# Kernel tuning notes

Hardware: AMD Instinct MI355X
Metric: run time of the kernel (lower is better)

Reference implementation:

```python
import jax, jax.numpy as jnp
import numpy as np

B, D_IN, H, LAT = 4096, 4096, 4096, 512


def setup_inputs() -> dict:
    key = jax.random.key(0)
    ks = jax.random.split(key, 10)
    s = lambda fan_in: 1.0 / np.sqrt(fan_in)
    return {
        "x": jax.random.normal(ks[0], (B, D_IN), jnp.float32),
        "W_e1": jax.random.normal(ks[1], (D_IN, H), jnp.float32) * s(D_IN),
        "b_e1": jax.random.uniform(ks[2], (H,), jnp.float32),
        "W_e2": jax.random.normal(ks[3], (H, 2 * LAT), jnp.float32) * s(H),
        "b_e2": jax.random.uniform(ks[4], (2 * LAT,), jnp.float32),
        "W_d1": jax.random.normal(ks[5], (LAT, H), jnp.float32) * s(LAT),
        "b_d1": jax.random.uniform(ks[6], (H,), jnp.float32),
        "W_d2": jax.random.normal(ks[7], (H, D_IN), jnp.float32) * s(H),
        "b_d2": jax.random.uniform(ks[8], (D_IN,), jnp.float32),
        "eps": jax.random.normal(ks[9], (B, LAT), jnp.float32),
    }


def reference(x, W_e1, b_e1, W_e2, b_e2, W_d1, b_d1, W_d2, b_d2, eps):
    # encoder MLP
    h = jax.nn.relu(x @ W_e1 + b_e1)
    z = h @ W_e2 + b_e2                      # [B, 2*LAT]
    mu, logvar = z[:, :LAT], z[:, LAT:]
    # reparameterize: cholesky(diag(exp(logvar))) @ eps + mu == exp(0.5*logvar)*eps + mu
    zs = mu + jnp.exp(0.5 * logvar) * eps    # [B, LAT]
    # decoder MLP
    hd = jax.nn.relu(zs @ W_d1 + b_d1)
    recon = hd @ W_d2 + b_d2                 # [B, D_IN]
    return recon, mu, logvar
```

## Files before the change

### kernel.cpp

```cpp
#include <hip/hip_runtime.h>
#include <hip/hip_bf16.h>

typedef __attribute__((ext_vector_type(8))) __bf16 bf16x8;
typedef __attribute__((ext_vector_type(4))) float f32x4;
typedef __attribute__((ext_vector_type(4))) unsigned short ushort4v;
typedef unsigned short u16;

__device__ __forceinline__ u16 f2bf_bits(float f) {
    union { float f; unsigned int u; } x; x.f = f;
    unsigned int r = x.u + 0x7FFFu + ((x.u >> 16) & 1u);
    return (u16)(r >> 16);
}

__device__ __forceinline__ void gload_lds16(const void* g, void* l) {
    __builtin_amdgcn_global_load_lds(
        (const __attribute__((address_space(1))) void*)g,
        (__attribute__((address_space(3))) void*)l, 16, 0, 0);
}

#define BARRIER()  __builtin_amdgcn_s_barrier()
#define LGKM0()    asm volatile("s_waitcnt lgkmcnt(0)" ::: "memory")
#define VMW8()     asm volatile("s_waitcnt vmcnt(8)" ::: "memory")

__global__ void cvt4(const float* __restrict__ in, u16* __restrict__ out, int n) {
    int i = (blockIdx.x * 256 + threadIdx.x) << 2;
    if (i >= n) return;
    f32x4 v = *reinterpret_cast<const f32x4*>(in + i);
    ushort4v o;
    o.x = f2bf_bits(v.x); o.y = f2bf_bits(v.y);
    o.z = f2bf_bits(v.z); o.w = f2bf_bits(v.w);
    *reinterpret_cast<ushort4v*>(out + i) = o;
}

__global__ __launch_bounds__(256)
void transpose_cvt64(const float* __restrict__ in, u16* __restrict__ out,
                     int R, int C) {
    __shared__ float t[64][67];
    const int c0 = blockIdx.x << 6;
    const int r0 = blockIdx.y << 6;
    const int tx = threadIdx.x & 15;
    const int ty = threadIdx.x >> 4;
    #pragma unroll
    for (int j = 0; j < 4; ++j) {
        f32x4 v = *reinterpret_cast<const f32x4*>(
            &in[(size_t)(r0 + ty + 16 * j) * C + c0 + (tx << 2)]);
        *reinterpret_cast<f32x4*>(&t[ty + 16 * j][tx << 2]) = v;
    }
    __syncthreads();
    const int oc = threadIdx.x >> 2;
    const int rr = (threadIdx.x & 3) << 2;
    #pragma unroll
    for (int j = 0; j < 4; ++j) {
        const int r = rr + 16 * j;
        ushort4v o;
        o.x = f2bf_bits(t[r + 0][oc]);
        o.y = f2bf_bits(t[r + 1][oc]);
        o.z = f2bf_bits(t[r + 2][oc]);
        o.w = f2bf_bits(t[r + 3][oc]);
        *reinterpret_cast<ushort4v*>(&out[(size_t)(c0 + oc) * R + r0 + r]) = o;
    }
}

__global__ void sampler(const float* __restrict__ mu, const float* __restrict__ lv,
                        const float* __restrict__ eps, u16* __restrict__ zs, int n) {
    int i = blockIdx.x * 256 + threadIdx.x;
    if (i >= n) return;
    float v = mu[i] + __expf(0.5f * lv[i]) * eps[i];
    zs[i] = f2bf_bits(v);
}

template<int MODE>
__global__ __launch_bounds__(256)
void gemm_bt(const u16* __restrict__ A, const u16* __restrict__ Bt,
             const float* __restrict__ bias,
             u16* __restrict__ obf, float* __restrict__ of32, float* __restrict__ olv,
             int M, int N, int K)
{
    __shared__ u16 As[128 * 32];
    __shared__ u16 Bs[128 * 32];

    const int tid  = threadIdx.x;
    const int lane = tid & 63;
    const int w    = tid >> 6;
    const int wr   = w >> 1;
    const int wc   = w & 1;

    const int nbx  = N >> 7;
    const int brow = (blockIdx.x / nbx) << 7;
    const int bcol = (blockIdx.x % nbx) << 7;

    const int srow = (w << 4) + (lane >> 2);
    const int scol = (lane & 3) << 3;
    const size_t aoff0 = (size_t)(brow + srow) * K + scol;
    const size_t aoff1 = (size_t)(brow + 64 + srow) * K + scol;
    const size_t boff0 = (size_t)(bcol + srow) * K + scol;
    const size_t boff1 = (size_t)(bcol + 64 + srow) * K + scol;

    u16* asl0 = &As[(w << 9)];
    u16* asl1 = &As[2048 + (w << 9)];
    u16* bsl0 = &Bs[(w << 9)];
    u16* bsl1 = &Bs[2048 + (w << 9)];

    f32x4 acc[4][4];
    #pragma unroll
    for (int m = 0; m < 4; ++m)
        #pragma unroll
        for (int n = 0; n < 4; ++n)
            acc[m][n] = (f32x4)(0.0f);

    const int ar   = (wr << 6) + (lane & 15);
    const int br   = (wc << 6) + (lane & 15);
    const int koff = (lane >> 4) << 3;

    for (int kt = 0; kt < K; kt += 32) {
        __syncthreads();
        gload_lds16(A  + aoff0 + kt, asl0);
        gload_lds16(A  + aoff1 + kt, asl1);
        gload_lds16(Bt + boff0 + kt, bsl0);
        gload_lds16(Bt + boff1 + kt, bsl1);
        __syncthreads();

        bf16x8 av[4], bv[4];
        #pragma unroll
        for (int m = 0; m < 4; ++m)
            av[m] = *reinterpret_cast<const bf16x8*>(&As[(ar + (m << 4)) * 32 + koff]);
        #pragma unroll
        for (int n = 0; n < 4; ++n)
            bv[n] = *reinterpret_cast<const bf16x8*>(&Bs[(br + (n << 4)) * 32 + koff]);

        #pragma unroll
        for (int m = 0; m < 4; ++m)
            #pragma unroll
            for (int n = 0; n < 4; ++n)
                acc[m][n] = __builtin_amdgcn_mfma_f32_16x16x32_bf16(
                    av[m], bv[n], acc[m][n], 0, 0, 0);
    }

    float bv4[4];
    #pragma unroll
    for (int n = 0; n < 4; ++n)
        bv4[n] = bias[bcol + (wc << 6) + (n << 4) + (lane & 15)];

    const int erow0 = brow + (wr << 6) + ((lane >> 4) << 2);
    const int ecol0 = bcol + (wc << 6) + (lane & 15);

    #pragma unroll
    for (int m = 0; m < 4; ++m) {
        #pragma unroll
        for (int i = 0; i < 4; ++i) {
            const int r = erow0 + (m << 4) + i;
            #pragma unroll
            for (int n = 0; n < 4; ++n) {
                const int c = ecol0 + (n << 4);
                float v = acc[m][n][i] + bv4[n];
                if (MODE == 0) {
                    v = v > 0.0f ? v : 0.0f;
                    obf[(size_t)r * N + c] = f2bf_bits(v);
                } else if (MODE == 1) {
                    of32[(size_t)r * N + c] = v;
                } else {
                    if (c < 512) of32[(size_t)r * 512 + c] = v;
                    else         olv[(size_t)r * 512 + (c - 512)] = v;
                }
            }
        }
    }
}

template<int MODE>
__global__ __launch_bounds__(512, 2)
void gemm256(const u16* __restrict__ A, const u16* __restrict__ Bt,
             const float* __restrict__ bias,
             u16* __restrict__ obf, float* __restrict__ of32,
             int M, int N, int K)
{
    extern __shared__ char lds[];
    const int tid  = threadIdx.x;
    const int lane = tid & 63;
    const int w    = tid >> 6;
    const int wr   = w >> 2;
    const int wc   = w & 3;

    int bid = blockIdx.x;
    const int cpx = gridDim.x >> 3;
    bid = (bid & 7) * cpx + (bid >> 3);
    const int nbx  = N >> 8;
    const int brow = (bid / nbx) << 8;
    const int bcol = (bid % nbx) << 8;

    const int srow  = tid >> 3;
    const int scole = (((tid & 7) ^ (srow & 7)) << 4) >> 1;
    const size_t aoff = (size_t)(brow + srow) * K + scole;
    const size_t boff = (size_t)(bcol + srow) * K + scole;
    const size_t rowK64 = (size_t)64 * K;
    const int wave1024 = w << 10;

    const int lo16 = (lane >> 4) << 4;
    const int swzm = (lane & 7) << 4;
    const int low0 = lo16 ^ swzm;
    const int low1 = (64 | lo16) ^ swzm;
    const int rA   = (lane & 15) << 7;
    const int rB   = ((((wc & 1) << 6) | (lane & 15)) << 7);
    const int regA = wr << 14;
    const int regB = 32768 + ((wc >> 1) << 14);

    bf16x8 a[4][2];
    bf16x8 b0[2][2];
    bf16x8 b1[2][2];
    f32x4 acc[8][4];
    #pragma unroll
    for (int m = 0; m < 8; ++m)
        #pragma unroll
        for (int n = 0; n < 4; ++n)
            acc[m][n] = (f32x4)(0.0f);

#define STAGE_A(buf, h, kt) do { \
    const u16* _s = A + aoff + (size_t)(h) * 128 * K + (size_t)(kt) * 64; \
    gload_lds16(_s,          lds + ((buf) << 16) + ((h) << 14) + wave1024); \
    gload_lds16(_s + rowK64, lds + ((buf) << 16) + ((h) << 14) + 8192 + wave1024); \
} while (0)

#define STAGE_B(buf, h, kt) do { \
    const u16* _s = Bt + boff + (size_t)(h) * 128 * K + (size_t)(kt) * 64; \
    gload_lds16(_s,          lds + ((buf) << 16) + 32768 + ((h) << 14) + wave1024); \
    gload_lds16(_s + rowK64, lds + ((buf) << 16) + 32768 + ((h) << 14) + 8192 + wave1024); \
} while (0)

#define READ_A(buf, g) do { \
    _Pragma("unroll") \
    for (int m = 0; m < 4; ++m) { \
        const int _b = ((buf) << 16) + regA + rA + ((((g) << 2) + m) << 11); \
        a[m][0] = *reinterpret_cast<const bf16x8*>(lds + _b + low0); \
        a[m][1] = *reinterpret_cast<const bf16x8*>(lds + _b + low1); \
    } \
} while (0)

#define READ_B0(buf) do { \
    _Pragma("unroll") \
    for (int n = 0; n < 2; ++n) { \
        const int _b = ((buf) << 16) + regB + rB + (n << 11); \
        b0[n][0] = *reinterpret_cast<const bf16x8*>(lds + _b + low0); \
        b0[n][1] = *reinterpret_cast<const bf16x8*>(lds + _b + low1); \
    } \
} while (0)

#define READ_B1(buf) do { \
    _Pragma("unroll") \
    for (int n = 0; n < 2; ++n) { \
        const int _b = ((buf) << 16) + regB + rB + ((n + 2) << 11); \
        b1[n][0] = *reinterpret_cast<const bf16x8*>(lds + _b + low0); \
        b1[n][1] = *reinterpret_cast<const bf16x8*>(lds + _b + low1); \
    } \
} while (0)

#define MM(bx, mb, nb) do { \
    __builtin_amdgcn_s_setprio(1); \
    _Pragma("unroll") \
    for (int m = 0; m < 4; ++m) \
        _Pragma("unroll") \
        for (int n = 0; n < 2; ++n) \
            _Pragma("unroll") \
            for (int s = 0; s < 2; ++s) \
                acc[(mb) + m][(nb) + n] = __builtin_amdgcn_mfma_f32_16x16x32_bf16( \
                    a[m][s], bx[n][s], acc[(mb) + m][(nb) + n], 0, 0, 0); \
    __builtin_amdgcn_s_setprio(0); \
} while (0)

    const int NT  = K >> 6;
    const int NIT = K >> 7;

    STAGE_A(0, 0, 0); STAGE_A(0, 1, 0); STAGE_B(0, 0, 0); STAGE_B(0, 1, 0);
    STAGE_A(1, 0, 1); STAGE_A(1, 1, 1); STAGE_B(1, 0, 1); STAGE_B(1, 1, 1);
    VMW8(); BARRIER();
    READ_A(0, 0); READ_B0(0);

    for (int it = 0; it < NIT; ++it) {
        const int tn0r = 2 * it + 2;
        const int tn1r = 2 * it + 3;
        const int tn0 = tn0r < NT ? tn0r : NT - 1;
        const int tn1 = tn1r < NT ? tn1r : NT - 1;

        BARRIER(); LGKM0();
        MM(b0, 0, 0);
        READ_B1(0);

        BARRIER(); LGKM0();
        STAGE_B(0, 0, tn0);
        MM(b1, 0, 2);
        READ_A(0, 1);

        BARRIER(); LGKM0();
        STAGE_B(0, 1, tn0);
        MM(b1, 4, 2);

        BARRIER(); LGKM0();
        STAGE_A(0, 0, tn0); STAGE_A(0, 1, tn0);
        MM(b0, 4, 0);
        VMW8();
        READ_A(1, 0); READ_B0(1);

        BARRIER(); LGKM0();
        MM(b0, 0, 0);
        READ_B1(1);

        BARRIER(); LGKM0();
        STAGE_B(1, 0, tn1);
        MM(b1, 0, 2);
        READ_A(1, 1);

        BARRIER(); LGKM0();
        STAGE_B(1, 1, tn1);
        MM(b1, 4, 2);

        BARRIER(); LGKM0();
        STAGE_A(1, 0, tn1); STAGE_A(1, 1, tn1);
        MM(b0, 4, 0);
        VMW8();
        READ_A(0, 0); READ_B0(0);
    }

    float bb[4];
    #pragma unroll
    for (int n = 0; n < 4; ++n)
        bb[n] = bias[bcol + (wc << 6) + (n << 4) + (lane & 15)];

    const int erow0 = brow + (wr << 7) + ((lane >> 4) << 2);
    const int ecol0 = bcol + (wc << 6) + (lane & 15);

    #pragma unroll
    for (int m = 0; m < 8; ++m) {
        #pragma unroll
        for (int i = 0; i < 4; ++i) {
            const int r = erow0 + (m << 4) + i;
            #pragma unroll
            for (int n = 0; n < 4; ++n) {
                const int c = ecol0 + (n << 4);
                float v = acc[m][n][i] + bb[n];
                if (MODE == 0) {
                    v = v > 0.0f ? v : 0.0f;
                    obf[(size_t)r * N + c] = f2bf_bits(v);
                } else {
                    of32[(size_t)r * N + c] = v;
                }
            }
        }
    }
#undef STAGE_A
#undef STAGE_B
#undef READ_A
#undef READ_B0
#undef READ_B1
#undef MM
}

extern "C" void kernel_launch(void* const* d_in, const int* in_sizes, int n_in,
                              void* d_out, int out_size, void* d_ws, size_t ws_size,
                              hipStream_t stream) {
    const float* x   = (const float*)d_in[0];
    const float* We1 = (const float*)d_in[1];
    const float* be1 = (const float*)d_in[2];
    const float* We2 = (const float*)d_in[3];
    const float* be2 = (const float*)d_in[4];
    const float* Wd1 = (const float*)d_in[5];
    const float* bd1 = (const float*)d_in[6];
    const float* Wd2 = (const float*)d_in[7];
    const float* bd2 = (const float*)d_in[8];
    const float* eps = (const float*)d_in[9];

    const int B = 4096, D = 4096, H = 4096, LAT = 512;

    char* ws = (char*)d_ws;
    u16* xb  = (u16*)(ws);
    u16* w1t = (u16*)(ws + 33554432);
    u16* w2t = (u16*)(ws + 67108864);
    u16* w3t = (u16*)(ws + 75497472);
    u16* w4t = (u16*)(ws + 79691776);
    u16* h   = (u16*)(ws + 113246208);
    u16* zs  = w1t;
    u16* hd  = xb;

    float* recon = (float*)d_out;
    float* mu    = recon + (size_t)B * D;
    float* lv    = mu + (size_t)B * LAT;

    hipFuncSetAttribute(reinterpret_cast<const void*>(gemm256<0>),
                        hipFuncAttributeMaxDynamicSharedMemorySize, 131072);
    hipFuncSetAttribute(reinterpret_cast<const void*>(gemm256<1>),
                        hipFuncAttributeMaxDynamicSharedMemorySize, 131072);

    cvt4<<<(B * D / 4 + 255) / 256, 256, 0, stream>>>(x, xb, B * D);
    transpose_cvt64<<<dim3(H / 64, D / 64), 256, 0, stream>>>(We1, w1t, D, H);
    transpose_cvt64<<<dim3(2 * LAT / 64, H / 64), 256, 0, stream>>>(We2, w2t, H, 2 * LAT);
    transpose_cvt64<<<dim3(H / 64, LAT / 64), 256, 0, stream>>>(Wd1, w3t, LAT, H);
    transpose_cvt64<<<dim3(D / 64, H / 64), 256, 0, stream>>>(Wd2, w4t, H, D);

    gemm256<0><<<(B / 256) * (H / 256), 512, 131072, stream>>>(xb, w1t, be1, h, nullptr, B, H, D);
    gemm_bt<2><<<(B / 128) * (2 * LAT / 128), 256, 0, stream>>>(h, w2t, be2, nullptr, mu, lv, B, 2 * LAT, H);
    sampler<<<(B * LAT + 255) / 256, 256, 0, stream>>>(mu, lv, eps, zs, B * LAT);
    gemm256<0><<<(B / 256) * (H / 256), 512, 131072, stream>>>(zs, w3t, bd1, hd, nullptr, B, H, LAT);
    gemm256<1><<<(B / 256) * (D / 256), 512, 131072, stream>>>(hd, w4t, bd2, nullptr, recon, B, D, H);
}
```

Measured before the change: 414.6 us.

## Replace 8-phase interleaved GEMM main loop with simple double-buffered tile loop

Replaces the finely interleaved 8-phase main loop, which had a barrier and an LDS wait per phase and issued partial stages, with a one-tile-per-iteration double-buffered loop. Each iteration issues the whole next tile's global->LDS loads up front, computes the current tile, then does a full vmcnt(0) wait and barrier before reading the next fragments. This cuts the number of barriers and waits per tile but makes the global-load wait coarser, which may expose memory latency that the staggered schedule hid. The explicit lgkmcnt waits are dropped, so the compiler must place the LDS read waits itself.

```diff
diff --git a/kernel.cpp b/kernel.cpp
--- a/kernel.cpp
+++ b/kernel.cpp
@@ -19,8 +19,7 @@
 }
 
 #define BARRIER()  __builtin_amdgcn_s_barrier()
-#define LGKM0()    asm volatile("s_waitcnt lgkmcnt(0)" ::: "memory")
-#define VMW8()     asm volatile("s_waitcnt vmcnt(8)" ::: "memory")
+#define VMW0()     asm volatile("s_waitcnt vmcnt(0)" ::: "memory")
 
 __global__ void cvt4(const float* __restrict__ in, u16* __restrict__ out, int n) {
     int i = (blockIdx.x * 256 + threadIdx.x) << 2;
@@ -266,57 +265,32 @@
     __builtin_amdgcn_s_setprio(0); \
 } while (0)
 
-    const int NT  = K >> 6;
-    const int NIT = K >> 7;
+    const int NT = K >> 6;
 
     STAGE_A(0, 0, 0); STAGE_A(0, 1, 0); STAGE_B(0, 0, 0); STAGE_B(0, 1, 0);
-    STAGE_A(1, 0, 1); STAGE_A(1, 1, 1); STAGE_B(1, 0, 1); STAGE_B(1, 1, 1);
-    VMW8(); BARRIER();
-    READ_A(0, 0); READ_B0(0);
-
-    for (int it = 0; it < NIT; ++it) {
-        const int tn0r = 2 * it + 2;
-        const int tn1r = 2 * it + 3;
-        const int tn0 = tn0r < NT ? tn0r : NT - 1;
-        const int tn1 = tn1r < NT ? tn1r : NT - 1;
-
-        BARRIER(); LGKM0();
+    VMW0(); BARRIER();
+    READ_A(0, 0); READ_B0(0); READ_B1(0);
+
+    for (int t = 0; t < NT; ++t) {
+        const int c  = t & 1;
+        const int cn = c ^ 1;
+        const int tn = (t + 1 < NT) ? t + 1 : NT - 1;
+
+        BARRIER();
+        STAGE_A(cn, 0, tn); STAGE_A(cn, 1, tn);
+        STAGE_B(cn, 0, tn); STAGE_B(cn, 1, tn);
+
         MM(b0, 0, 0);
-        READ_B1(0);
-
-        BARRIER(); LGKM0();
-        STAGE_B(0, 0, tn0);
         MM(b1, 0, 2);
-        READ_A(0, 1);
-
-        BARRIER(); LGKM0();
-        STAGE_B(0, 1, tn0);
+        READ_A(c, 1);
+        MM(b0, 4, 0);
+
+        VMW0();
+        BARRIER();
+
+        READ_B0(cn);
         MM(b1, 4, 2);
-
-        BARRIER(); LGKM0();
-        STAGE_A(0, 0, tn0); STAGE_A(0, 1, tn0);
-        MM(b0, 4, 0);
-        VMW8();
-        READ_A(1, 0); READ_B0(1);
-
-        BARRIER(); LGKM0();
-        MM(b0, 0, 0);
-        READ_B1(1);
-
-        BARRIER(); LGKM0();
-        STAGE_B(1, 0, tn1);
-        MM(b1, 0, 2);
-        READ_A(1, 1);
-
-        BARRIER(); LGKM0();
-        STAGE_B(1, 1, tn1);
-        MM(b1, 4, 2);
-
-        BARRIER(); LGKM0();
-        STAGE_A(1, 0, tn1); STAGE_A(1, 1, tn1);
-        MM(b0, 4, 0);
-        VMW8();
-        READ_A(0, 0); READ_B0(0);
+        READ_A(cn, 0); READ_B1(cn);
     }
 
     float bb[4];
```

New measurement: 434.7 us. +4.9%, slower.

## Split-K the encoder second GEMM on the 256-tile kernel and fuse reduction with sampler

Applied to the files above, without the earlier changes.

The old 128-tile gemm_bt for h@W_e2 (N=1024) is replaced by the pipelined gemm256 in a new split-K mode. Each of four K slices writes fp32 partials to workspace. A new zred kernel sums the partials, adds the bias, writes mu and logvar, and computes the reparameterized bf16 zs in one pass, replacing the separate sampler. This targets low occupancy (only 64 tiles of 256 without split-K) and the weaker old kernel, at the cost of extra partial-sum traffic of about 64MB write plus read.

```diff
diff --git a/kernel.cpp b/kernel.cpp
--- a/kernel.cpp
+++ b/kernel.cpp
@@ -61,110 +61,37 @@
     }
 }
 
-__global__ void sampler(const float* __restrict__ mu, const float* __restrict__ lv,
-                        const float* __restrict__ eps, u16* __restrict__ zs, int n) {
-    int i = blockIdx.x * 256 + threadIdx.x;
-    if (i >= n) return;
-    float v = mu[i] + __expf(0.5f * lv[i]) * eps[i];
-    zs[i] = f2bf_bits(v);
-}
-
-template<int MODE>
 __global__ __launch_bounds__(256)
-void gemm_bt(const u16* __restrict__ A, const u16* __restrict__ Bt,
-             const float* __restrict__ bias,
-             u16* __restrict__ obf, float* __restrict__ of32, float* __restrict__ olv,
-             int M, int N, int K)
-{
-    __shared__ u16 As[128 * 32];
-    __shared__ u16 Bs[128 * 32];
-
-    const int tid  = threadIdx.x;
-    const int lane = tid & 63;
-    const int w    = tid >> 6;
-    const int wr   = w >> 1;
-    const int wc   = w & 1;
-
-    const int nbx  = N >> 7;
-    const int brow = (blockIdx.x / nbx) << 7;
-    const int bcol = (blockIdx.x % nbx) << 7;
-
-    const int srow = (w << 4) + (lane >> 2);
-    const int scol = (lane & 3) << 3;
-    const size_t aoff0 = (size_t)(brow + srow) * K + scol;
-    const size_t aoff1 = (size_t)(brow + 64 + srow) * K + scol;
-    const size_t boff0 = (size_t)(bcol + srow) * K + scol;
-    const size_t boff1 = (size_t)(bcol + 64 + srow) * K + scol;
-
-    u16* asl0 = &As[(w << 9)];
-    u16* asl1 = &As[2048 + (w << 9)];
-    u16* bsl0 = &Bs[(w << 9)];
-    u16* bsl1 = &Bs[2048 + (w << 9)];
-
-    f32x4 acc[4][4];
-    #pragma unroll
-    for (int m = 0; m < 4; ++m)
-        #pragma unroll
-        for (int n = 0; n < 4; ++n)
-            acc[m][n] = (f32x4)(0.0f);
-
-    const int ar   = (wr << 6) + (lane & 15);
-    const int br   = (wc << 6) + (lane & 15);
-    const int koff = (lane >> 4) << 3;
-
-    for (int kt = 0; kt < K; kt += 32) {
-        __syncthreads();
-        gload_lds16(A  + aoff0 + kt, asl0);
-        gload_lds16(A  + aoff1 + kt, asl1);
-        gload_lds16(Bt + boff0 + kt, bsl0);
-        gload_lds16(Bt + boff1 + kt, bsl1);
-        __syncthreads();
-
-        bf16x8 av[4], bv[4];
-        #pragma unroll
-        for (int m = 0; m < 4; ++m)
-            av[m] = *reinterpret_cast<const bf16x8*>(&As[(ar + (m << 4)) * 32 + koff]);
-        #pragma unroll
-        for (int n = 0; n < 4; ++n)
-            bv[n] = *reinterpret_cast<const bf16x8*>(&Bs[(br + (n << 4)) * 32 + koff]);
-
-        #pragma unroll
-        for (int m = 0; m < 4; ++m)
-            #pragma unroll
-            for (int n = 0; n < 4; ++n)
-                acc[m][n] = __builtin_amdgcn_mfma_f32_16x16x32_bf16(
-                    av[m], bv[n], acc[m][n], 0, 0, 0);
-    }
-
-    float bv4[4];
-    #pragma unroll
-    for (int n = 0; n < 4; ++n)
-        bv4[n] = bias[bcol + (wc << 6) + (n << 4) + (lane & 15)];
-
-    const int erow0 = brow + (wr << 6) + ((lane >> 4) << 2);
-    const int ecol0 = bcol + (wc << 6) + (lane & 15);
-
-    #pragma unroll
-    for (int m = 0; m < 4; ++m) {
-        #pragma unroll
-        for (int i = 0; i < 4; ++i) {
-            const int r = erow0 + (m << 4) + i;
-            #pragma unroll
-            for (int n = 0; n < 4; ++n) {
-                const int c = ecol0 + (n << 4);
-                float v = acc[m][n][i] + bv4[n];
-                if (MODE == 0) {
-                    v = v > 0.0f ? v : 0.0f;
-                    obf[(size_t)r * N + c] = f2bf_bits(v);
-                } else if (MODE == 1) {
-                    of32[(size_t)r * N + c] = v;
-                } else {
-                    if (c < 512) of32[(size_t)r * 512 + c] = v;
-                    else         olv[(size_t)r * 512 + (c - 512)] = v;
-                }
-            }
-        }
-    }
+void zred(const float* __restrict__ P, const float* __restrict__ be2,
+          const float* __restrict__ eps, float* __restrict__ mu,
+          float* __restrict__ lv, u16* __restrict__ zs) {
+    const int i = blockIdx.x * 256 + threadIdx.x;
+    const int r = i >> 7;
+    const int c4 = (i & 127) << 2;
+    const size_t base = (size_t)r * 1024 + c4;
+    const size_t PS = (size_t)4096 * 1024;
+
+    f32x4 m = *reinterpret_cast<const f32x4*>(P + base);
+    f32x4 l = *reinterpret_cast<const f32x4*>(P + base + 512);
+    #pragma unroll
+    for (int s = 1; s < 4; ++s) {
+        m += *reinterpret_cast<const f32x4*>(P + s * PS + base);
+        l += *reinterpret_cast<const f32x4*>(P + s * PS + base + 512);
+    }
+    m += *reinterpret_cast<const f32x4*>(be2 + c4);
+    l += *reinterpret_cast<const f32x4*>(be2 + 512 + c4);
+
+    const size_t ob = (size_t)r * 512 + c4;
+    *reinterpret_cast<f32x4*>(mu + ob) = m;
+    *reinterpret_cast<f32x4*>(lv + ob) = l;
+
+    f32x4 e = *reinterpret_cast<const f32x4*>(eps + ob);
+    ushort4v o;
+    o.x = f2bf_bits(m.x + __expf(0.5f * l.x) * e.x);
+    o.y = f2bf_bits(m.y + __expf(0.5f * l.y) * e.y);
+    o.z = f2bf_bits(m.z + __expf(0.5f * l.z) * e.z);
+    o.w = f2bf_bits(m.w + __expf(0.5f * l.w) * e.w);
+    *reinterpret_cast<ushort4v*>(zs + ob) = o;
 }
 
 template<int MODE>
@@ -172,7 +99,7 @@
 void gemm256(const u16* __restrict__ A, const u16* __restrict__ Bt,
              const float* __restrict__ bias,
              u16* __restrict__ obf, float* __restrict__ of32,
-             int M, int N, int K)
+             int M, int N, int K, int ntiles)
 {
     extern __shared__ char lds[];
     const int tid  = threadIdx.x;
@@ -182,11 +109,16 @@
     const int wc   = w & 3;
 
     int bid = blockIdx.x;
-    const int cpx = gridDim.x >> 3;
+    int sid = 0;
+    int nwg = gridDim.x;
+    if (MODE == 3) { sid = bid & 3; bid >>= 2; nwg >>= 2; }
+    const int cpx = nwg >> 3;
     bid = (bid & 7) * cpx + (bid >> 3);
     const int nbx  = N >> 8;
     const int brow = (bid / nbx) << 8;
     const int bcol = (bid % nbx) << 8;
+    const int kbase = (MODE == 3) ? sid * ntiles : 0;
+    float* pout = (MODE == 3) ? of32 + (size_t)sid * M * N : of32;
 
     const int srow  = tid >> 3;
     const int scole = (((tid & 7) ^ (srow & 7)) << 4) >> 1;
@@ -266,19 +198,18 @@
     __builtin_amdgcn_s_setprio(0); \
 } while (0)
 
-    const int NT  = K >> 6;
-    const int NIT = K >> 7;
-
-    STAGE_A(0, 0, 0); STAGE_A(0, 1, 0); STAGE_B(0, 0, 0); STAGE_B(0, 1, 0);
-    STAGE_A(1, 0, 1); STAGE_A(1, 1, 1); STAGE_B(1, 0, 1); STAGE_B(1, 1, 1);
+    const int NIT = ntiles >> 1;
+
+    STAGE_A(0, 0, kbase); STAGE_A(0, 1, kbase); STAGE_B(0, 0, kbase); STAGE_B(0, 1, kbase);
+    STAGE_A(1, 0, kbase + 1); STAGE_A(1, 1, kbase + 1); STAGE_B(1, 0, kbase + 1); STAGE_B(1, 1, kbase + 1);
     VMW8(); BARRIER();
     READ_A(0, 0); READ_B0(0);
 
     for (int it = 0; it < NIT; ++it) {
         const int tn0r = 2 * it + 2;
         const int tn1r = 2 * it + 3;
-        const int tn0 = tn0r < NT ? tn0r : NT - 1;
-        const int tn1 = tn1r < NT ? tn1r : NT - 1;
+        const int tn0 = kbase + (tn0r < ntiles ? tn0r : ntiles - 1);
+        const int tn1 = kbase + (tn1r < ntiles ? tn1r : ntiles - 1);
 
         BARRIER(); LGKM0();
         MM(b0, 0, 0);
@@ -322,7 +253,7 @@
     float bb[4];
     #pragma unroll
     for (int n = 0; n < 4; ++n)
-        bb[n] = bias[bcol + (wc << 6) + (n << 4) + (lane & 15)];
+        bb[n] = (MODE == 3) ? 0.0f : bias[bcol + (wc << 6) + (n << 4) + (lane & 15)];
 
     const int erow0 = brow + (wr << 7) + ((lane >> 4) << 2);
     const int ecol0 = bcol + (wc << 6) + (lane & 15);
@@ -340,7 +271,7 @@
                     v = v > 0.0f ? v : 0.0f;
                     obf[(size_t)r * N + c] = f2bf_bits(v);
                 } else {
-                    of32[(size_t)r * N + c] = v;
+                    pout[(size_t)r * N + c] = v;
                 }
             }
         }
@@ -370,14 +301,15 @@
     const int B = 4096, D = 4096, H = 4096, LAT = 512;
 
     char* ws = (char*)d_ws;
-    u16* xb  = (u16*)(ws);
-    u16* w1t = (u16*)(ws + 33554432);
-    u16* w2t = (u16*)(ws + 67108864);
-    u16* w3t = (u16*)(ws + 75497472);
-    u16* w4t = (u16*)(ws + 79691776);
-    u16* h   = (u16*)(ws + 113246208);
-    u16* zs  = w1t;
-    u16* hd  = xb;
+    u16*   xb   = (u16*)(ws);
+    u16*   w1t  = (u16*)(ws + 33554432);
+    u16*   w2t  = (u16*)(ws + 67108864);
+    u16*   w3t  = (u16*)(ws + 75497472);
+    u16*   w4t  = (u16*)(ws + 79691776);
+    u16*   h    = (u16*)(ws + 113246208);
+    float* part = (float*)(ws);
+    u16*   zs   = (u16*)(ws + 113246208);
+    u16*   hd   = (u16*)(ws);
 
     float* recon = (float*)d_out;
     float* mu    = recon + (size_t)B * D;
@@ -386,6 +318,8 @@
     hipFuncSetAttribute(reinterpret_cast<const void*>(gemm256<0>),
                         hipFuncAttributeMaxDynamicSharedMemorySize, 131072);
     hipFuncSetAttribute(reinterpret_cast<const void*>(gemm256<1>),
+                        hipFuncAttributeMaxDynamicSharedMemorySize, 131072);
+    hipFuncSetAttribute(reinterpret_cast<const void*>(gemm256<3>),
                         hipFuncAttributeMaxDynamicSharedMemorySize, 131072);
 
     cvt4<<<(B * D / 4 + 255) / 256, 256, 0, stream>>>(x, xb, B * D);
@@ -394,9 +328,13 @@
     transpose_cvt64<<<dim3(H / 64, LAT / 64), 256, 0, stream>>>(Wd1, w3t, LAT, H);
     transpose_cvt64<<<dim3(D / 64, H / 64), 256, 0, stream>>>(Wd2, w4t, H, D);
 
-    gemm256<0><<<(B / 256) * (H / 256), 512, 131072, stream>>>(xb, w1t, be1, h, nullptr, B, H, D);
-    gemm_bt<2><<<(B / 128) * (2 * LAT / 128), 256, 0, stream>>>(h, w2t, be2, nullptr, mu, lv, B, 2 * LAT, H);
-    sampler<<<(B * LAT + 255) / 256, 256, 0, stream>>>(mu, lv, eps, zs, B * LAT);
-    gemm256<0><<<(B / 256) * (H / 256), 512, 131072, stream>>>(zs, w3t, bd1, hd, nullptr, B, H, LAT);
-    gemm256<1><<<(B / 256) * (D / 256), 512, 131072, stream>>>(hd, w4t, bd2, nullptr, recon, B, D, H);
-}
+    gemm256<0><<<(B / 256) * (H / 256), 512, 131072, stream>>>(
+        xb, w1t, be1, h, nullptr, B, H, D, D / 64);
+    gemm256<3><<<(B / 256) * (2 * LAT / 256) * 4, 512, 131072, stream>>>(
+        h, w2t, nullptr, nullptr, part, B, 2 * LAT, H, (H / 64) / 4);
+    zred<<<(B * LAT / 4) / 256, 256, 0, stream>>>(part, be2, eps, mu, lv, zs);
+    gemm256<0><<<(B / 256) * (H / 256), 512, 131072, stream>>>(
+        zs, w3t, bd1, hd, nullptr, B, H, LAT, LAT / 64);
+    gemm256<1><<<(B / 256) * (D / 256), 512, 131072, stream>>>(
+        hd, w4t, bd2, nullptr, recon, B, D, H, H / 64);
+}
```

After: 371.9 us. -10.3%, faster.
